# Kernel tuning notes

Hardware: AMD Instinct MI355X
Metric: run time of the kernel (lower is better)

## Reference

```python
import jax, jax.numpy as jnp
import numpy as np

DIM = 128
WS = 7          # window size
NH = 4          # num heads
N = WS * WS     # tokens per window = 49
GRID = 56       # 224/4 token grid -> 8x8 = 64 windows per image
NUM_WIN = (GRID // WS) ** 2  # 64
IMG_B = 64
SCALE = (DIM // NH) ** -0.5


def _relative_position_index():
    coords = np.stack(np.meshgrid(np.arange(WS), np.arange(WS), indexing='ij'))  # (2,WS,WS)
    flat = coords.reshape(2, -1)                         # (2, N)
    rel = flat[:, :, None] - flat[:, None, :]            # (2, N, N)
    rel = rel.transpose(1, 2, 0).astype(np.int32)        # (N, N, 2)
    rel[:, :, 0] += WS - 1
    rel[:, :, 1] += WS - 1
    rel[:, :, 0] *= 2 * WS - 1
    return jnp.asarray(rel.sum(-1))                      # (N, N) int32


def _shift_mask():
    # Swin shifted-window attention mask: shift = WS // 2, off-group pairs get -100.
    shift = WS // 2
    img = np.zeros((GRID, GRID), dtype=np.int32)
    cnt = 0
    segs = (slice(0, -WS), slice(-WS, -shift), slice(-shift, None))
    for hs in segs:
        for ws_ in segs:
            img[hs, ws_] = cnt
            cnt += 1
    # window partition -> (NUM_WIN, N)
    w = img.reshape(GRID // WS, WS, GRID // WS, WS).transpose(0, 2, 1, 3).reshape(NUM_WIN, N)
    diff = w[:, :, None] - w[:, None, :]
    return jnp.asarray(np.where(diff != 0, -100.0, 0.0).astype(np.float32))  # (NUM_WIN, N, N)


def setup_inputs() -> dict:
    key = jax.random.key(0)
    ks = jax.random.split(key, 6)
    B = IMG_B * NUM_WIN  # 4096
    x = jax.random.normal(ks[0], (B, N, DIM), dtype=jnp.float32)
    qkv_w = jax.random.normal(ks[1], (3 * DIM, DIM), dtype=jnp.float32) * (DIM ** -0.5)
    qkv_b = jnp.zeros((3 * DIM,), dtype=jnp.float32)
    proj_w = jax.random.normal(ks[2], (DIM, DIM), dtype=jnp.float32) * (DIM ** -0.5)
    proj_b = jnp.zeros((DIM,), dtype=jnp.float32)
    rel_bias_table = jax.random.normal(ks[3], ((2 * WS - 1) ** 2, NH), dtype=jnp.float32) * 0.02
    return {
        'x': x,
        'mask': _shift_mask(),
        'qkv_w': qkv_w,
        'qkv_b': qkv_b,
        'proj_w': proj_w,
        'proj_b': proj_b,
        'rel_bias_table': rel_bias_table,
        'rel_index': _relative_position_index(),
    }


def reference(x, mask, qkv_w, qkv_b, proj_w, proj_b, rel_bias_table, rel_index):
    B, n, C = x.shape
    hd = C // NH
    qkv = (x @ qkv_w.T + qkv_b).reshape(B, n, 3, NH, hd)
    q = qkv[:, :, 0].transpose(0, 2, 1, 3) * SCALE   # (B, H, N, hd)
    k = qkv[:, :, 1].transpose(0, 2, 1, 3)
    v = qkv[:, :, 2].transpose(0, 2, 1, 3)
    attn = jnp.einsum('bhnd,bhmd->bhnm', q, k)       # (B, H, N, N)
    bias = rel_bias_table[rel_index.reshape(-1)].reshape(n, n, NH).transpose(2, 0, 1)
    attn = attn + bias[None]
    nW = mask.shape[0]
    attn = attn.reshape(B // nW, nW, NH, n, n) + mask[None, :, None]
    attn = jax.nn.softmax(attn.reshape(B, NH, n, n), axis=-1)
    out = jnp.einsum('bhnm,bhmd->bhnd', attn, v).transpose(0, 2, 1, 3).reshape(B, n, C)
    return out @ proj_w.T + proj_b
```

## Files before the change

kernel.cpp:

```cpp
#include <hip/hip_runtime.h>


#define NTOK  49
#define DIMC  128
#define NBLK  4096
#define SCALE 0.17677669529663687f
#define LOG2E 1.4426950408889634f
#define NMASK -144.26950408889634f

typedef __attribute__((ext_vector_type(8))) short bf16x8;
typedef __attribute__((ext_vector_type(4))) float f32x4;

#define WS_QKVW 0
#define WS_PROJW 49152
#define WS_BIAS  65536
#define WS_TOTAL 81920

#define PS_OFF    0
#define PS_G      3528
#define PS_STRIDE 72
#define XS_STRIDE 136
#define QS_OFF    7056
#define QS_HB     2080
#define QS_STRIDE 40
#define KS_OFF    15376
#define VT_OFF    23696
#define VT_STRIDE 72
#define SMEM_TOT  32912

__device__ __forceinline__ unsigned int pkbf2(float f0, float f1) {
    union { float f; unsigned int i; } a, b; a.f = f0; b.f = f1;
    return __builtin_amdgcn_perm(b.i + 0x8000u, a.i + 0x8000u, 0x07060302u);
}
__device__ __forceinline__ unsigned short f2b_r(float f) {
    union { float f; unsigned int i; } v; v.f = f;
    return (unsigned short)((v.i + 0x8000u) >> 16);
}
__device__ __forceinline__ float b2f_lo(unsigned int u) {
    union { unsigned int i; float f; } v; v.i = u << 16; return v.f;
}
__device__ __forceinline__ float b2f_hi(unsigned int u) {
    union { unsigned int i; float f; } v; v.i = u & 0xFFFF0000u; return v.f;
}
__device__ __forceinline__ float exp2_hw(float x) {
    float r; asm("v_exp_f32 %0, %1" : "=v"(r) : "v"(x)); return r;
}

__device__ __forceinline__ int seg3(int c) { return (c < 49) ? 0 : ((c < 53) ? 1 : 2); }

__global__ __launch_bounds__(256)
void prep(const float* __restrict__ qkv_w, const float* __restrict__ proj_w,
          const float* __restrict__ bias_t, const int* __restrict__ rel_idx,
          unsigned short* __restrict__ ws)
{
    int idx = blockIdx.x * 256 + threadIdx.x;
    if (idx < 8192) {
        int base = idx * 8;
        const float* sp = (base < 49152) ? (qkv_w + base) : (proj_w + (base - 49152));
        float sc = (base < 16384) ? (SCALE * LOG2E) : 1.0f;
        float4 a = *(const float4*)sp;
        float4 b = *(const float4*)(sp + 4);
        uint4 u;
        u.x = pkbf2(a.x * sc, a.y * sc);
        u.y = pkbf2(a.z * sc, a.w * sc);
        u.z = pkbf2(b.x * sc, b.y * sc);
        u.w = pkbf2(b.z * sc, b.w * sc);
        *(uint4*)(ws + base) = u;
    } else {
        int i = idx - 8192;
        int reg = i & 3, lane = (i >> 2) & 63, nt = (i >> 8) & 3,
            mt = (i >> 10) & 3, h = (i >> 12) & 3;
        int row = mt * 16 + (lane >> 4) * 4 + reg;
        int col = nt * 16 + (lane & 15);
        float v = 0.f;
        if (row < NTOK && col < NTOK)
            v = bias_t[rel_idx[row * NTOK + col] * 4 + h] * LOG2E;
        ws[WS_BIAS + i] = f2b_r(v);
    }
}

__global__ __launch_bounds__(512, 4)
void win_attn(const float* __restrict__ x,
              const float* __restrict__ qkv_b,
              const float* __restrict__ proj_b,
              const unsigned short* __restrict__ ws,
              float* __restrict__ out)
{
    __shared__ unsigned short smem[SMEM_TOT];
    const int b    = blockIdx.x;
    const int w    = b & 63;
    const int tid  = threadIdx.x;
    const int wv   = tid >> 6;
    const int lane = tid & 63;
    const int qg   = lane >> 4;
    const int l15  = lane & 15;

    {
        const float4* xg = (const float4*)(x + (size_t)b * (NTOK * DIMC));
        #pragma unroll
        for (int it = 0; it < 4; it++) {
            int i = tid + it * 512;
            if (i < NTOK * DIMC / 4) {
                float4 v = xg[i];
                int row = i >> 5, col = (i & 31) * 4;
                uint2 u; u.x = pkbf2(v.x, v.y); u.y = pkbf2(v.z, v.w);
                *(uint2*)(smem + PS_OFF + row * XS_STRIDE + col) = u;
            }
        }
        if (tid < 384) {
            int hz = tid / 96;
            int rem = tid - hz * 96;
            int rowz = NTOK + (rem >> 5);
            int dz = rem & 31;
            smem[KS_OFF + hz * QS_HB + rowz * QS_STRIDE + dz] = 0;
        }
    }
    __syncthreads();

    bf16x8 af[4][4];
    #pragma unroll
    for (int mt = 0; mt < 4; mt++) {
        int ar = mt * 16 + l15; if (ar > 48) ar = 48;
        #pragma unroll
        for (int ks_ = 0; ks_ < 4; ks_++)
            af[mt][ks_] = *(const bf16x8*)(smem + PS_OFF + ar * XS_STRIDE + ks_ * 32 + qg * 8);
    }

    {
        const unsigned short* qw = ws + WS_QKVW;
        const int h2 = wv >> 1;
        const int dh = (wv & 1) * 16 + l15;
        #pragma unroll
        for (int pp = 0; pp < 3; pp++) {
            const int j = (pp * 8 + wv) * 16 + l15;
            bf16x8 bfr[4];
            #pragma unroll
            for (int ks_ = 0; ks_ < 4; ks_++)
                bfr[ks_] = *(const bf16x8*)(qw + j * DIMC + ks_ * 32 + qg * 8);
            const float bias = (pp == 0) ? qkv_b[j] * (SCALE * LOG2E) : qkv_b[j];
            #pragma unroll
            for (int mt = 0; mt < 4; mt++) {
                f32x4 acc = { bias, bias, bias, bias };
                #pragma unroll
                for (int ks_ = 0; ks_ < 4; ks_++)
                    acc = __builtin_amdgcn_mfma_f32_16x16x32_bf16(af[mt][ks_], bfr[ks_], acc, 0, 0, 0);
                if (pp == 0) {
                    #pragma unroll
                    for (int r = 0; r < 4; r++) {
                        int row = mt * 16 + qg * 4 + r;
                        if (row < NTOK)
                            smem[QS_OFF + h2 * QS_HB + row * QS_STRIDE + dh] = f2b_r(acc[r]);
                    }
                } else if (pp == 1) {
                    #pragma unroll
                    for (int r = 0; r < 4; r++) {
                        int row = mt * 16 + qg * 4 + r;
                        if (row < NTOK)
                            smem[KS_OFF + h2 * QS_HB + row * QS_STRIDE + dh] = f2b_r(acc[r]);
                    }
                } else {
                    uint2 u; u.x = pkbf2(acc[0], acc[1]); u.y = pkbf2(acc[2], acc[3]);
                    *(uint2*)(smem + VT_OFF + (h2 * 32 + dh) * VT_STRIDE + mt * 16 + qg * 4) = u;
                }
            }
        }
    }
    __syncthreads();

    const int g  = wv >> 2;
    const int st = wv & 3;
    const int r0 = st * 16;
    const int wy = w >> 3, wx = w & 7;
    float mreg[4][4];
    {
        int grow[4];
        #pragma unroll
        for (int r = 0; r < 4; r++) {
            int t = r0 + qg * 4 + r;
            int ty = (t * 9363) >> 16, tx = t - ty * 7;
            grow[r] = seg3(wy * 7 + ty) * 3 + seg3(wx * 7 + tx);
        }
        #pragma unroll
        for (int nt = 0; nt < 4; nt++) {
            int t = nt * 16 + l15;
            int ty = (t * 9363) >> 16, tx = t - ty * 7;
            int gcol = seg3(wy * 7 + ty) * 3 + seg3(wx * 7 + tx);
            bool vc = t < NTOK;
            #pragma unroll
            for (int r = 0; r < 4; r++)
                mreg[nt][r] = !vc ? -1e30f : ((grow[r] == gcol) ? 0.f : NMASK);
        }
    }
    int ar2 = r0 + l15; if (ar2 > 48) ar2 = 48;

    #pragma unroll
    for (int hh = 0; hh < 2; hh++) {
        const int h = g * 2 + hh;
        const bf16x8 aq = *(const bf16x8*)(smem + QS_OFF + h * QS_HB + ar2 * QS_STRIDE + qg * 8);
        float sv[4][4];
        #pragma unroll
        for (int nt = 0; nt < 4; nt++) {
            bf16x8 bk = *(const bf16x8*)(smem + KS_OFF + h * QS_HB + (nt * 16 + l15) * QS_STRIDE + qg * 8);
            f32x4 z = { 0.f, 0.f, 0.f, 0.f };
            f32x4 c = __builtin_amdgcn_mfma_f32_16x16x32_bf16(aq, bk, z, 0, 0, 0);
            uint2 bb = *(const uint2*)(ws + WS_BIAS + (((h * 4 + st) * 4 + nt) * 64 + lane) * 4);
            sv[nt][0] = c[0] + b2f_lo(bb.x) + mreg[nt][0];
            sv[nt][1] = c[1] + b2f_hi(bb.x) + mreg[nt][1];
            sv[nt][2] = c[2] + b2f_lo(bb.y) + mreg[nt][2];
            sv[nt][3] = c[3] + b2f_hi(bb.y) + mreg[nt][3];
        }
        float p[4][4], inv[4];
        #pragma unroll
        for (int r = 0; r < 4; r++) {
            float mx = fmaxf(fmaxf(sv[0][r], sv[1][r]), fmaxf(sv[2][r], sv[3][r]));
            mx = fmaxf(mx, __shfl_xor(mx, 1));
            mx = fmaxf(mx, __shfl_xor(mx, 2));
            mx = fmaxf(mx, __shfl_xor(mx, 4));
            mx = fmaxf(mx, __shfl_xor(mx, 8));
            float sum = 0.f;
            #pragma unroll
            for (int nt = 0; nt < 4; nt++) {
                float e = exp2_hw(sv[nt][r] - mx);
                p[nt][r] = e; sum += e;
            }
            sum += __shfl_xor(sum, 1);
            sum += __shfl_xor(sum, 2);
            sum += __shfl_xor(sum, 4);
            sum += __shfl_xor(sum, 8);
            inv[r] = __builtin_amdgcn_rcpf(sum);
        }
        #pragma unroll
        for (int nt = 0; nt < 4; nt++)
            #pragma unroll
            for (int r = 0; r < 4; r++) {
                int row = r0 + qg * 4 + r;
                if (row < NTOK)
                    smem[PS_OFF + g * PS_G + row * PS_STRIDE + nt * 16 + l15] = f2b_r(p[nt][r]);
            }
        f32x4 accO[2] = { { 0.f, 0.f, 0.f, 0.f }, { 0.f, 0.f, 0.f, 0.f } };
        #pragma unroll
        for (int ks2 = 0; ks2 < 2; ks2++) {
            bf16x8 ap = *(const bf16x8*)(smem + PS_OFF + g * PS_G + ar2 * PS_STRIDE + ks2 * 32 + qg * 8);
            #pragma unroll
            for (int nt2 = 0; nt2 < 2; nt2++) {
                bf16x8 bvv = *(const bf16x8*)(smem + VT_OFF + (h * 32 + nt2 * 16 + l15) * VT_STRIDE + ks2 * 32 + qg * 8);
                accO[nt2] = __builtin_amdgcn_mfma_f32_16x16x32_bf16(ap, bvv, accO[nt2], 0, 0, 0);
            }
        }
        #pragma unroll
        for (int nt2 = 0; nt2 < 2; nt2++)
            #pragma unroll
            for (int r = 0; r < 4; r++) {
                int row = r0 + qg * 4 + r;
                if (row < NTOK)
                    smem[QS_OFF + h * QS_HB + row * QS_STRIDE + nt2 * 16 + l15] =
                        f2b_r(accO[nt2][r] * inv[r]);
            }
    }
    __syncthreads();

    {
        const int mt = wv & 3, jh = wv >> 2;
        int ar = mt * 16 + l15; if (ar > 48) ar = 48;
        bf16x8 ad[4];
        #pragma unroll
        for (int ks_ = 0; ks_ < 4; ks_++)
            ad[ks_] = *(const bf16x8*)(smem + QS_OFF + ks_ * QS_HB + ar * QS_STRIDE + qg * 8);
        const unsigned short* pw = ws + WS_PROJW;
        float* ob = out + (size_t)b * (NTOK * DIMC);
        #pragma unroll
        for (int jt2 = 0; jt2 < 4; jt2++) {
            const int j = jh * 64 + jt2 * 16 + l15;
            bf16x8 bfr[4];
            #pragma unroll
            for (int ks_ = 0; ks_ < 4; ks_++)
                bfr[ks_] = *(const bf16x8*)(pw + j * DIMC + ks_ * 32 + qg * 8);
            const float pb = proj_b[j];
            f32x4 acc = { pb, pb, pb, pb };
            #pragma unroll
            for (int ks_ = 0; ks_ < 4; ks_++)
                acc = __builtin_amdgcn_mfma_f32_16x16x32_bf16(ad[ks_], bfr[ks_], acc, 0, 0, 0);
            #pragma unroll
            for (int r = 0; r < 4; r++) {
                int row = mt * 16 + qg * 4 + r;
                if (row < NTOK) ob[row * DIMC + j] = acc[r];
            }
        }
    }
}

extern "C" void kernel_launch(void* const* d_in, const int* in_sizes, int n_in,
                              void* d_out, int out_size, void* d_ws, size_t ws_size,
                              hipStream_t stream) {
    const float* x      = (const float*)d_in[0];
    const float* qkv_w  = (const float*)d_in[2];
    const float* qkv_b  = (const float*)d_in[3];
    const float* proj_w = (const float*)d_in[4];
    const float* proj_b = (const float*)d_in[5];
    const float* bias_t = (const float*)d_in[6];
    const int*   relidx = (const int*)d_in[7];
    float*       outp   = (float*)d_out;
    unsigned short* ws  = (unsigned short*)d_ws;

    prep<<<96, 256, 0, stream>>>(qkv_w, proj_w, bias_t, relidx, ws);
    win_attn<<<NBLK, 512, 0, stream>>>(x, qkv_b, proj_b, ws, outp);
}
```

Measured before the change: 300.6 us.

## Compact shared-memory layout by aliasing Q/P/O buffers and fragment-ordering V

New measurement: 420.2 us. 1.4x slower.

```diff
diff --git a/kernel.cpp b/kernel.cpp
--- a/kernel.cpp
+++ b/kernel.cpp
@@ -14,19 +14,12 @@
 #define WS_QKVW 0
 #define WS_PROJW 49152
 #define WS_BIAS  65536
-#define WS_TOTAL 81920
-
-#define PS_OFF    0
-#define PS_G      3528
-#define PS_STRIDE 72
-#define XS_STRIDE 136
-#define QS_OFF    7056
-#define QS_HB     2080
-#define QS_STRIDE 40
-#define KS_OFF    15376
-#define VT_OFF    23696
-#define VT_STRIDE 72
-#define SMEM_TOT  32912
+
+#define QP_OFF    0
+#define QP_STRIDE 136
+#define K_OFF     6664
+#define VB_OFF    13328
+#define SMEM_TOT  21520
 
 __device__ __forceinline__ unsigned int pkbf2(float f0, float f1) {
     union { float f; unsigned int i; } a, b; a.f = f0; b.f = f1;
@@ -79,7 +72,7 @@
     }
 }
 
-__global__ __launch_bounds__(512, 4)
+__global__ __launch_bounds__(512, 6)
 void win_attn(const float* __restrict__ x,
               const float* __restrict__ qkv_b,
               const float* __restrict__ proj_b,
@@ -104,15 +97,8 @@
                 float4 v = xg[i];
                 int row = i >> 5, col = (i & 31) * 4;
                 uint2 u; u.x = pkbf2(v.x, v.y); u.y = pkbf2(v.z, v.w);
-                *(uint2*)(smem + PS_OFF + row * XS_STRIDE + col) = u;
-            }
-        }
-        if (tid < 384) {
-            int hz = tid / 96;
-            int rem = tid - hz * 96;
-            int rowz = NTOK + (rem >> 5);
-            int dz = rem & 31;
-            smem[KS_OFF + hz * QS_HB + rowz * QS_STRIDE + dz] = 0;
+                *(uint2*)(smem + QP_OFF + row * QP_STRIDE + col) = u;
+            }
         }
     }
     __syncthreads();
@@ -123,13 +109,15 @@
         int ar = mt * 16 + l15; if (ar > 48) ar = 48;
         #pragma unroll
         for (int ks_ = 0; ks_ < 4; ks_++)
-            af[mt][ks_] = *(const bf16x8*)(smem + PS_OFF + ar * XS_STRIDE + ks_ * 32 + qg * 8);
-    }
+            af[mt][ks_] = *(const bf16x8*)(smem + QP_OFF + ar * QP_STRIDE + ks_ * 32 + qg * 8);
+    }
+    __syncthreads();
 
     {
         const unsigned short* qw = ws + WS_QKVW;
         const int h2 = wv >> 1;
-        const int dh = (wv & 1) * 16 + l15;
+        const int dhalf = wv & 1;
+        const int dh = dhalf * 16 + l15;
         #pragma unroll
         for (int pp = 0; pp < 3; pp++) {
             const int j = (pp * 8 + wv) * 16 + l15;
@@ -149,18 +137,22 @@
                     for (int r = 0; r < 4; r++) {
                         int row = mt * 16 + qg * 4 + r;
                         if (row < NTOK)
-                            smem[QS_OFF + h2 * QS_HB + row * QS_STRIDE + dh] = f2b_r(acc[r]);
+                            smem[QP_OFF + row * QP_STRIDE + h2 * 32 + dh] = f2b_r(acc[r]);
                     }
                 } else if (pp == 1) {
                     #pragma unroll
                     for (int r = 0; r < 4; r++) {
                         int row = mt * 16 + qg * 4 + r;
                         if (row < NTOK)
-                            smem[KS_OFF + h2 * QS_HB + row * QS_STRIDE + dh] = f2b_r(acc[r]);
+                            smem[K_OFF + row * QP_STRIDE + h2 * 32 + dh] = f2b_r(acc[r]);
                     }
                 } else {
+                    int ks2 = mt >> 1;
+                    int qgp = (mt & 1) * 2 + (qg >> 1);
+                    int j0  = (qg & 1) * 4;
                     uint2 u; u.x = pkbf2(acc[0], acc[1]); u.y = pkbf2(acc[2], acc[3]);
-                    *(uint2*)(smem + VT_OFF + (h2 * 32 + dh) * VT_STRIDE + mt * 16 + qg * 4) = u;
+                    *(uint2*)(smem + VB_OFF + h2 * 2048 + ks2 * 1024 + dhalf * 512
+                              + qgp * 128 + l15 * 8 + j0) = u;
                 }
             }
         }
@@ -171,45 +163,45 @@
     const int st = wv & 3;
     const int r0 = st * 16;
     const int wy = w >> 3, wx = w & 7;
-    float mreg[4][4];
-    {
-        int grow[4];
-        #pragma unroll
-        for (int r = 0; r < 4; r++) {
-            int t = r0 + qg * 4 + r;
-            int ty = (t * 9363) >> 16, tx = t - ty * 7;
-            grow[r] = seg3(wy * 7 + ty) * 3 + seg3(wx * 7 + tx);
-        }
+    int grow[4];
+    #pragma unroll
+    for (int r = 0; r < 4; r++) {
+        int t = r0 + qg * 4 + r;
+        int ty = (t * 9363) >> 16, tx = t - ty * 7;
+        grow[r] = seg3(wy * 7 + ty) * 3 + seg3(wx * 7 + tx);
+    }
+    int arq = r0 + l15; if (arq > 48) arq = 48;
+
+    const bf16x8 aq0 = *(const bf16x8*)(smem + QP_OFF + arq * QP_STRIDE + (2 * g) * 32 + qg * 8);
+    const bf16x8 aq1 = *(const bf16x8*)(smem + QP_OFF + arq * QP_STRIDE + (2 * g + 1) * 32 + qg * 8);
+
+    f32x4 accO[2][2] = { { {0.f,0.f,0.f,0.f}, {0.f,0.f,0.f,0.f} },
+                         { {0.f,0.f,0.f,0.f}, {0.f,0.f,0.f,0.f} } };
+
+    #pragma unroll
+    for (int hh = 0; hh < 2; hh++) {
+        const int h = 2 * g + hh;
+        const bf16x8 aq = hh ? aq1 : aq0;
+        float sv[4][4];
         #pragma unroll
         for (int nt = 0; nt < 4; nt++) {
+            int krow = nt * 16 + l15; if (krow > 48) krow = 48;
+            bf16x8 bk = *(const bf16x8*)(smem + K_OFF + krow * QP_STRIDE + h * 32 + qg * 8);
+            f32x4 z = { 0.f, 0.f, 0.f, 0.f };
+            f32x4 c = __builtin_amdgcn_mfma_f32_16x16x32_bf16(aq, bk, z, 0, 0, 0);
+            uint2 bb = *(const uint2*)(ws + WS_BIAS + (((h * 4 + st) * 4 + nt) * 64 + lane) * 4);
             int t = nt * 16 + l15;
             int ty = (t * 9363) >> 16, tx = t - ty * 7;
             int gcol = seg3(wy * 7 + ty) * 3 + seg3(wx * 7 + tx);
             bool vc = t < NTOK;
-            #pragma unroll
-            for (int r = 0; r < 4; r++)
-                mreg[nt][r] = !vc ? -1e30f : ((grow[r] == gcol) ? 0.f : NMASK);
-        }
-    }
-    int ar2 = r0 + l15; if (ar2 > 48) ar2 = 48;
-
-    #pragma unroll
-    for (int hh = 0; hh < 2; hh++) {
-        const int h = g * 2 + hh;
-        const bf16x8 aq = *(const bf16x8*)(smem + QS_OFF + h * QS_HB + ar2 * QS_STRIDE + qg * 8);
-        float sv[4][4];
-        #pragma unroll
-        for (int nt = 0; nt < 4; nt++) {
-            bf16x8 bk = *(const bf16x8*)(smem + KS_OFF + h * QS_HB + (nt * 16 + l15) * QS_STRIDE + qg * 8);
-            f32x4 z = { 0.f, 0.f, 0.f, 0.f };
-            f32x4 c = __builtin_amdgcn_mfma_f32_16x16x32_bf16(aq, bk, z, 0, 0, 0);
-            uint2 bb = *(const uint2*)(ws + WS_BIAS + (((h * 4 + st) * 4 + nt) * 64 + lane) * 4);
-            sv[nt][0] = c[0] + b2f_lo(bb.x) + mreg[nt][0];
-            sv[nt][1] = c[1] + b2f_hi(bb.x) + mreg[nt][1];
-            sv[nt][2] = c[2] + b2f_lo(bb.y) + mreg[nt][2];
-            sv[nt][3] = c[3] + b2f_hi(bb.y) + mreg[nt][3];
-        }
-        float p[4][4], inv[4];
+            float bv[4] = { b2f_lo(bb.x), b2f_hi(bb.x), b2f_lo(bb.y), b2f_hi(bb.y) };
+            #pragma unroll
+            for (int r = 0; r < 4; r++) {
+                float v = c[r] + bv[r] + ((grow[r] == gcol) ? 0.f : NMASK);
+                sv[nt][r] = vc ? v : -1e30f;
+            }
+        }
+        float inv[4];
         #pragma unroll
         for (int r = 0; r < 4; r++) {
             float mx = fmaxf(fmaxf(sv[0][r], sv[1][r]), fmaxf(sv[2][r], sv[3][r]));
@@ -221,7 +213,7 @@
             #pragma unroll
             for (int nt = 0; nt < 4; nt++) {
                 float e = exp2_hw(sv[nt][r] - mx);
-                p[nt][r] = e; sum += e;
+                sv[nt][r] = e; sum += e;
             }
             sum += __shfl_xor(sum, 1);
             sum += __shfl_xor(sum, 2);
@@ -235,28 +227,34 @@
             for (int r = 0; r < 4; r++) {
                 int row = r0 + qg * 4 + r;
                 if (row < NTOK)
-                    smem[PS_OFF + g * PS_G + row * PS_STRIDE + nt * 16 + l15] = f2b_r(p[nt][r]);
-            }
-        f32x4 accO[2] = { { 0.f, 0.f, 0.f, 0.f }, { 0.f, 0.f, 0.f, 0.f } };
+                    smem[QP_OFF + row * QP_STRIDE + g * 64 + nt * 16 + l15] = f2b_r(sv[nt][r]);
+            }
         #pragma unroll
         for (int ks2 = 0; ks2 < 2; ks2++) {
-            bf16x8 ap = *(const bf16x8*)(smem + PS_OFF + g * PS_G + ar2 * PS_STRIDE + ks2 * 32 + qg * 8);
+            bf16x8 ap = *(const bf16x8*)(smem + QP_OFF + arq * QP_STRIDE + g * 64 + ks2 * 32 + qg * 8);
             #pragma unroll
             for (int nt2 = 0; nt2 < 2; nt2++) {
-                bf16x8 bvv = *(const bf16x8*)(smem + VT_OFF + (h * 32 + nt2 * 16 + l15) * VT_STRIDE + ks2 * 32 + qg * 8);
-                accO[nt2] = __builtin_amdgcn_mfma_f32_16x16x32_bf16(ap, bvv, accO[nt2], 0, 0, 0);
-            }
-        }
+                bf16x8 bvv = *(const bf16x8*)(smem + VB_OFF + h * 2048 + ks2 * 1024 + nt2 * 512 + lane * 8);
+                accO[hh][nt2] = __builtin_amdgcn_mfma_f32_16x16x32_bf16(ap, bvv, accO[hh][nt2], 0, 0, 0);
+            }
+        }
+        #pragma unroll
+        for (int nt2 = 0; nt2 < 2; nt2++)
+            #pragma unroll
+            for (int r = 0; r < 4; r++)
+                accO[hh][nt2][r] *= inv[r];
+    }
+    #pragma unroll
+    for (int hh = 0; hh < 2; hh++)
         #pragma unroll
         for (int nt2 = 0; nt2 < 2; nt2++)
             #pragma unroll
             for (int r = 0; r < 4; r++) {
                 int row = r0 + qg * 4 + r;
                 if (row < NTOK)
-                    smem[QS_OFF + h * QS_HB + row * QS_STRIDE + nt2 * 16 + l15] =
-                        f2b_r(accO[nt2][r] * inv[r]);
-            }
-    }
+                    smem[QP_OFF + row * QP_STRIDE + (2 * g + hh) * 32 + nt2 * 16 + l15] =
+                        f2b_r(accO[hh][nt2][r]);
+            }
     __syncthreads();
 
     {
@@ -265,7 +263,7 @@
         bf16x8 ad[4];
         #pragma unroll
         for (int ks_ = 0; ks_ < 4; ks_++)
-            ad[ks_] = *(const bf16x8*)(smem + QS_OFF + ks_ * QS_HB + ar * QS_STRIDE + qg * 8);
+            ad[ks_] = *(const bf16x8*)(smem + QP_OFF + ar * QP_STRIDE + ks_ * 32 + qg * 8);
         const unsigned short* pw = ws + WS_PROJW;
         float* ob = out + (size_t)b * (NTOK * DIMC);
         #pragma unroll
```
